# Performance work log

Measured on AMD Instinct MI355X. Metric: run time of the kernel, lower is better.

The kernel has to match this reference:

```python
import jax, jax.numpy as jnp
import numpy as np
import math

B, S, E, H, FF = 2, 2048, 768, 12, 3072
D = E // H
SCALING = 1.0
EPS = 1e-5


def layer_norm(x, g, b):
    mu = jnp.mean(x, axis=-1, keepdims=True)
    var = jnp.var(x, axis=-1, keepdims=True)
    return (x - mu) * jax.lax.rsqrt(var + EPS) * g + b


def setup_inputs() -> dict:
    key = jax.random.key(0)
    ks = jax.random.split(key, 16)
    s_e = 1.0 / math.sqrt(E)
    s_f = 1.0 / math.sqrt(FF)
    inp = {
        "x": jax.random.normal(ks[0], (B, S, E), dtype=jnp.float32),
        "Wq": jax.random.uniform(ks[1], (E, E), jnp.float32, -s_e, s_e),
        "bq": jnp.zeros((E,), jnp.float32),
        "Wk": jax.random.uniform(ks[2], (E, E), jnp.float32, -s_e, s_e),
        "bk": jnp.zeros((E,), jnp.float32),
        "Wv": jax.random.uniform(ks[3], (E, E), jnp.float32, -s_e, s_e),
        "bv": jnp.zeros((E,), jnp.float32),
        "Wo": jax.random.uniform(ks[4], (E, E), jnp.float32, -s_e, s_e),
        "bo": jnp.zeros((E,), jnp.float32),
        "W1": jax.random.uniform(ks[5], (E, FF), jnp.float32, -s_e, s_e),
        "b1": jnp.zeros((FF,), jnp.float32),
        "W2": jax.random.uniform(ks[6], (FF, E), jnp.float32, -s_f, s_f),
        "b2": jnp.zeros((E,), jnp.float32),
        "g1": jnp.ones((E,), jnp.float32),
        "be1": jnp.zeros((E,), jnp.float32),
        "g2": jnp.ones((E,), jnp.float32),
        "be2": jnp.zeros((E,), jnp.float32),
    }
    return inp


def reference(x, Wq, bq, Wk, bk, Wv, bv, Wo, bo, W1, b1, W2, b2, g1, be1, g2, be2):
    # --- multi-head attention with ALiBi-style symmetric distance bias ---
    q = (x @ Wq + bq).reshape(B, S, H, D)
    k = (x @ Wk + bk).reshape(B, S, H, D)
    v = (x @ Wv + bv).reshape(B, S, H, D)
    scores = jnp.einsum("bqhd,bkhd->bhqk", q, k) / math.sqrt(D)
    pos = jnp.arange(S)
    alibi = -SCALING * jnp.abs(pos[None, :] - pos[:, None]).astype(jnp.float32)  # [S,S]
    scores = scores + alibi  # broadcast over [B,H]
    attn_map = jax.nn.softmax(scores, axis=-1)  # [B,H,S,S]
    ctx = jnp.einsum("bhqk,bkhd->bqhd", attn_map, v).reshape(B, S, E)
    attn_out = ctx @ Wo + bo
    # --- residual + norm, FFN, residual + norm (dropout = eval/identity) ---
    h = layer_norm(x + attn_out, g1, be1)
    ff = jax.nn.relu(h @ W1 + b1) @ W2 + b2
    out = layer_norm(h + ff, g2, be2)
    return (out, attn_map)
```

## Files before the change

### kernel.cpp

```cpp
#include <hip/hip_runtime.h>
#include <stdint.h>

static constexpr int cB = 2, cS = 2048, cE = 768, cH = 12, cFF = 3072, cD = 64;
static constexpr int cM = cB * cS;

typedef __bf16 bf16x8 __attribute__((ext_vector_type(8)));
typedef float f32x4 __attribute__((ext_vector_type(4)));

__device__ __forceinline__ unsigned short f2bf(float f) {
    union { float f; unsigned int u; } v; v.f = f;
    unsigned int r = v.u + 0x7fffu + ((v.u >> 16) & 1u);
    return (unsigned short)(r >> 16);
}
__device__ __forceinline__ float bf2f(unsigned short u) {
    union { unsigned int u; float f; } v; v.u = ((unsigned int)u) << 16;
    return v.f;
}

__device__ __forceinline__ void load_lds16(const unsigned short* g, unsigned short* l) {
    __builtin_amdgcn_global_load_lds(
        (const __attribute__((address_space(1))) unsigned int*)(g),
        (__attribute__((address_space(3))) unsigned int*)(l), 16, 0, 0);
}

static constexpr size_t ZTOT = 25165824;
static constexpr int ZPB = 9984;
static constexpr int ZPT = 39;

__device__ __forceinline__ void zstore_job(float* zattn, size_t j) {
    if (j < ZTOT) {
        int row  = (int)(j >> 9);
        int slot = (int)(j & 511);
        int m064 = (row & 2047) & ~63;
        int ntlo = (m064 > 120) ? ((m064 - 120) >> 7) : 0;
        int nthi = (m064 + 183) >> 7; if (nthi > 15) nthi = 15;
        int zlo = ntlo << 5;
        int span = ((nthi + 1) << 5) - zlo;
        int chunk = slot < zlo ? slot : slot + span;
        if (chunk < 512) {
            const f32x4 z4 = {0.f, 0.f, 0.f, 0.f};
            __builtin_nontemporal_store(z4, (f32x4*)zattn + ((size_t)row << 9) + chunk);
        }
    }
}

template<int BM, int BN, int EPI>
__global__ __launch_bounds__(256, 4) void gemm_nt(
    const unsigned short* __restrict__ Ab,
    const unsigned short* __restrict__ Btp,
    float* __restrict__ outF,
    float* __restrict__ outF2,
    unsigned short* __restrict__ outB,
    unsigned short* __restrict__ outB2,
    const float* __restrict__ bias0,
    const float* __restrict__ bias1,
    const float* __restrict__ bias2,
    const float* __restrict__ resid,
    float* __restrict__ zattn, int zbase, int zqs,
    int M, int N, int K, long sB)
{
    constexpr int MI = BM / 32, NI = BN / 32;
    __shared__ alignas(16) unsigned short Sh[BM * 64 + BN * 64];
    unsigned short* Al = Sh;
    unsigned short* Bl = Sh + BM * 64;
    const int tid = threadIdx.x;
    const int lane = tid & 63, wave = tid >> 6;
    const int wm = wave >> 1, wn = wave & 1;

    const int nwg  = gridDim.x * gridDim.y * gridDim.z;
    const int orig = blockIdx.x + gridDim.x * (blockIdx.y + gridDim.y * blockIdx.z);
    const int swz  = (orig & 7) * (nwg >> 3) + (orig >> 3);
    const int bx   = swz % gridDim.x;
    const int byz  = swz / gridDim.x;
    const int by   = byz % gridDim.y;
    const int bz   = byz / gridDim.y;

    const int m0 = by * BM, n0 = bx * BN;
    const int ln = lane & 15, lg = lane >> 4;
    const int sw = ln & 7;

    const unsigned short* Bt = Btp + (size_t)bz * sB;

    const size_t zb = (size_t)(zbase + orig) * ZPB;
    int zq0 = 0;

    f32x4 acc[MI][NI];
#pragma unroll
    for (int i = 0; i < MI; i++)
#pragma unroll
        for (int j = 0; j < NI; j++) acc[i][j] = (f32x4){0.f, 0.f, 0.f, 0.f};

    int kbeg = 0, kend = K;
    if constexpr (EPI == 3) { int kh = K >> 1; kbeg = bz * kh; kend = kbeg + kh; }

    for (int k0 = kbeg; k0 < kend; k0 += 64) {
        __syncthreads();
#pragma unroll
        for (int it = 0; it < BM / 32; ++it) {
            int idx = tid + it * 256;
            int r = idx >> 3, c8 = idx & 7;
            int cs = c8 ^ (r & 7);
            load_lds16(Ab + (size_t)(m0 + r) * K + k0 + cs * 8, &Al[idx * 8]);
        }
#pragma unroll
        for (int it = 0; it < BN / 32; ++it) {
            int idx = tid + it * 256;
            int r = idx >> 3, c8 = idx & 7;
            int cs = c8 ^ (r & 7);
            load_lds16(Bt + (size_t)(n0 + r) * K + k0 + cs * 8, &Bl[idx * 8]);
        }
        if (zattn) {
            for (int q = 0; q < zqs && (zq0 + q) < ZPT; ++q)
                zstore_job(zattn, zb + (size_t)(zq0 + q) * 256 + tid);
            zq0 += zqs;
        }
        __syncthreads();
#pragma unroll
        for (int ks = 0; ks < 2; ++ks) {
            bf16x8 av[MI], bv[NI];
#pragma unroll
            for (int i = 0; i < MI; i++) {
                int row = wm * (BM / 2) + 16 * i + ln;
                av[i] = *(const bf16x8*)&Al[row * 64 + ((ks * 4 + lg) ^ sw) * 8];
            }
#pragma unroll
            for (int j = 0; j < NI; j++) {
                int row = wn * (BN / 2) + 16 * j + ln;
                bv[j] = *(const bf16x8*)&Bl[row * 64 + ((ks * 4 + lg) ^ sw) * 8];
            }
#pragma unroll
            for (int i = 0; i < MI; i++)
#pragma unroll
                for (int j = 0; j < NI; j++)
                    acc[i][j] = __builtin_amdgcn_mfma_f32_16x16x32_bf16(av[i], bv[j], acc[i][j], 0, 0, 0);
        }
    }
    if (zattn) {
        for (; zq0 < ZPT; ++zq0)
            zstore_job(zattn, zb + (size_t)zq0 * 256 + tid);
    }

    if constexpr (EPI == 0) {
        if (bz < 2) {
            const float* bia = (bz == 0) ? bias0 : bias1;
#pragma unroll
            for (int i = 0; i < MI; i++)
#pragma unroll
                for (int j = 0; j < NI; j++)
#pragma unroll
                    for (int r = 0; r < 4; r++) {
                        int m = m0 + wm * (BM / 2) + 16 * i + lg * 4 + r;
                        int n = n0 + wn * (BN / 2) + 16 * j + ln;
                        float v = acc[i][j][r] + bia[n];
                        int b = m >> 11, s = m & 2047, h = n >> 6, d = n & 63;
                        outB[(size_t)bz * ((size_t)cB * cH * cS * cD) +
                             ((((size_t)b * cH + h) * cS + s) << 6) + d] = f2bf(v);
                    }
        } else {
            constexpr int TS = BM + 8;
            __syncthreads();
#pragma unroll
            for (int i = 0; i < MI; i++)
#pragma unroll
                for (int j = 0; j < NI; j++)
#pragma unroll
                    for (int r = 0; r < 4; r++) {
                        int ml = wm * (BM / 2) + 16 * i + lg * 4 + r;
                        int nl = wn * (BN / 2) + 16 * j + ln;
                        Sh[nl * TS + ml] = f2bf(acc[i][j][r] + bias2[n0 + nl]);
                    }
            __syncthreads();
            const int b = m0 >> 11, sbase = m0 & 2047;
#pragma unroll
            for (int it = 0; it < (BN * BM / 8) / 256; ++it) {
                int idx = tid + it * 256;
                int rr = idx >> 4, c8 = idx & 15;
                uint4 val = *(const uint4*)&Sh[rr * TS + c8 * 8];
                int ng = n0 + rr;
                int h = ng >> 6, d = ng & 63;
                *(uint4*)&outB2[((((size_t)b * cH + h) << 6) + d) * (size_t)cS + sbase + c8 * 8] = val;
            }
        }
    } else if constexpr (EPI == 3) {
        float* o = (bz == 0) ? outF : outF2;
#pragma unroll
        for (int i = 0; i < MI; i++) {
#pragma unroll
            for (int j = 0; j < NI; j++) {
#pragma unroll
                for (int r = 0; r < 4; r++) {
                    int m = m0 + wm * (BM / 2) + 16 * i + lg * 4 + r;
                    int n = n0 + wn * (BN / 2) + 16 * j + ln;
                    float v = acc[i][j][r];
                    if (bz == 0) v += bias0[n] + resid[(size_t)m * N + n];
                    o[(size_t)m * N + n] = v;
                }
            }
        }
    } else {
#pragma unroll
        for (int i = 0; i < MI; i++) {
#pragma unroll
            for (int j = 0; j < NI; j++) {
#pragma unroll
                for (int r = 0; r < 4; r++) {
                    int m = m0 + wm * (BM / 2) + 16 * i + lg * 4 + r;
                    int n = n0 + wn * (BN / 2) + 16 * j + ln;
                    float v = fmaxf(acc[i][j][r] + bias0[n], 0.f);
                    outB[(size_t)m * N + n] = f2bf(v);
                }
            }
        }
    }
}

__global__ __launch_bounds__(256, 2) void attn_fused(
    const unsigned short* __restrict__ Qh,
    const unsigned short* __restrict__ Kh,
    const unsigned short* __restrict__ Vt,
    float* __restrict__ attn,
    unsigned short* __restrict__ ctxb)
{
    constexpr int VS = 136;
    __shared__ alignas(16) unsigned short KVl[128 * 64];
    __shared__ alignas(16) unsigned short Pl[3 * 64 * VS];
    __shared__ float rs2[2][64];
    __shared__ float rsinv[64];

    const int tid = threadIdx.x;
    const int lane = tid & 63, wave = tid >> 6;
    const int wm = wave >> 1, wn = wave & 1;
    const int ln = lane & 15, lg = lane >> 4;
    const int sw = ln & 7;

    const int nwg  = gridDim.x * gridDim.y;
    const int orig = blockIdx.x + gridDim.x * blockIdx.y;
    const int swz  = (orig & 7) * (nwg >> 3) + (orig >> 3);
    const int m0 = (swz % gridDim.x) * 64;
    const int bh = swz / gridDim.x;

    const int nt_lo = max(0, (m0 - 120) / 128);
    const int nt_hi = min(15, (m0 + 183) / 128);

    const unsigned short* Qg = Qh + ((size_t)bh * cS + m0) * cD;
    const unsigned short* Kg = Kh + (size_t)bh * cS * cD;
    const unsigned short* Vg = Vt + (size_t)bh * cD * cS;
    float* attng = attn + (size_t)bh * cS * cS;

#pragma unroll
    for (int it = 0; it < 2; ++it) {
        int idx = tid + it * 256;
        int r = idx >> 3, c8 = idx & 7;
        int cs = c8 ^ (r & 7);
        load_lds16(Qg + r * cD + cs * 8, &KVl[idx * 8]);
    }
    __syncthreads();
    bf16x8 qf[2][2];
#pragma unroll
    for (int ks = 0; ks < 2; ++ks)
#pragma unroll
        for (int i = 0; i < 2; i++)
            qf[ks][i] = *(const bf16x8*)&KVl[(wm * 32 + 16 * i + ln) * 64 + ((ks * 4 + lg) ^ sw) * 8];

    float psum[8];
#pragma unroll
    for (int k = 0; k < 8; k++) psum[k] = 0.f;
    f32x4 oacc[2][2];
#pragma unroll
    for (int i = 0; i < 2; i++)
#pragma unroll
        for (int j = 0; j < 2; j++) oacc[i][j] = (f32x4){0.f, 0.f, 0.f, 0.f};

    for (int nt = nt_lo; nt <= nt_hi; ++nt) {
        unsigned short* Pb = &Pl[(nt - nt_lo) * 64 * VS];
        __syncthreads();
#pragma unroll
        for (int it = 0; it < 4; ++it) {
            int idx = tid + it * 256;
            int r = idx >> 3, c8 = idx & 7;
            int cs = c8 ^ (r & 7);
            load_lds16(Kg + (size_t)(nt * 128 + r) * cD + cs * 8, &KVl[idx * 8]);
        }
        __syncthreads();
        f32x4 acc[2][4];
#pragma unroll
        for (int i = 0; i < 2; i++)
#pragma unroll
            for (int j = 0; j < 4; j++) acc[i][j] = (f32x4){0.f, 0.f, 0.f, 0.f};
#pragma unroll
        for (int ks = 0; ks < 2; ++ks) {
            bf16x8 b[4];
#pragma unroll
            for (int j = 0; j < 4; j++)
                b[j] = *(const bf16x8*)&KVl[(wn * 64 + 16 * j + ln) * 64 + ((ks * 4 + lg) ^ sw) * 8];
            __builtin_amdgcn_s_setprio(1);
#pragma unroll
            for (int i = 0; i < 2; i++)
#pragma unroll
                for (int j = 0; j < 4; j++)
                    acc[i][j] = __builtin_amdgcn_mfma_f32_16x16x32_bf16(qf[ks][i], b[j], acc[i][j], 0, 0, 0);
            __builtin_amdgcn_s_setprio(0);
        }
#pragma unroll
        for (int i = 0; i < 2; i++)
#pragma unroll
            for (int j = 0; j < 4; j++)
#pragma unroll
                for (int r = 0; r < 4; r++) {
                    int mloc = wm * 32 + 16 * i + lg * 4 + r;
                    int nloc = wn * 64 + 16 * j + ln;
                    int mg = m0 + mloc, ng = nt * 128 + nloc;
                    float e = __expf(acc[i][j][r] * 0.125f - fabsf((float)(mg - ng)));
                    psum[i * 4 + r] += e;
                    Pb[mloc * VS + nloc] = f2bf(e);
                }
        __syncthreads();
#pragma unroll
        for (int it = 0; it < 4; ++it) {
            int idx = tid + it * 256;
            int r = idx >> 4, c8 = idx & 15;
            int cs = c8 ^ (r & 7);
            load_lds16(Vg + (size_t)r * cS + nt * 128 + cs * 8, &KVl[idx * 8]);
        }
        __syncthreads();
#pragma unroll
        for (int ks = 0; ks < 4; ++ks) {
            bf16x8 pa[2], vb[2];
#pragma unroll
            for (int i = 0; i < 2; i++)
                pa[i] = *(const bf16x8*)&Pb[(wm * 32 + 16 * i + ln) * VS + ks * 32 + lg * 8];
#pragma unroll
            for (int j = 0; j < 2; j++) {
                int row = wn * 32 + 16 * j + ln;
                vb[j] = *(const bf16x8*)&KVl[row * 128 + ((ks * 4 + lg) ^ sw) * 8];
            }
            __builtin_amdgcn_s_setprio(1);
#pragma unroll
            for (int i = 0; i < 2; i++)
#pragma unroll
                for (int j = 0; j < 2; j++)
                    oacc[i][j] = __builtin_amdgcn_mfma_f32_16x16x32_bf16(pa[i], vb[j], oacc[i][j], 0, 0, 0);
            __builtin_amdgcn_s_setprio(0);
        }
    }

#pragma unroll
    for (int k = 0; k < 8; k++) {
        float v = psum[k];
        v += __shfl_xor(v, 1); v += __shfl_xor(v, 2);
        v += __shfl_xor(v, 4); v += __shfl_xor(v, 8);
        psum[k] = v;
    }
    if (ln == 0) {
#pragma unroll
        for (int i = 0; i < 2; i++)
#pragma unroll
            for (int r = 0; r < 4; r++)
                rs2[wn][wm * 32 + 16 * i + lg * 4 + r] = psum[i * 4 + r];
    }
    __syncthreads();
    if (tid < 64) rsinv[tid] = 1.f / (rs2[0][tid] + rs2[1][tid]);
    __syncthreads();
    float invl[8];
#pragma unroll
    for (int i = 0; i < 2; i++)
#pragma unroll
        for (int r = 0; r < 4; r++)
            invl[i * 4 + r] = rsinv[wm * 32 + 16 * i + lg * 4 + r];

    {
        int b = bh / cH, h = bh % cH;
#pragma unroll
        for (int i = 0; i < 2; i++)
#pragma unroll
            for (int j = 0; j < 2; j++)
#pragma unroll
                for (int r = 0; r < 4; r++) {
                    int mg = m0 + wm * 32 + 16 * i + lg * 4 + r;
                    int d = wn * 32 + 16 * j + ln;
                    ctxb[((size_t)b * cS + mg) * cE + h * 64 + d] = f2bf(oacc[i][j][r] * invl[i * 4 + r]);
                }
    }
    for (int nt = nt_lo; nt <= nt_hi; ++nt) {
        const unsigned short* Pb = &Pl[(nt - nt_lo) * 64 * VS];
#pragma unroll
        for (int t = 0; t < 8; ++t) {
            int idx = t * 256 + tid;
            int row = idx >> 5, c4 = idx & 31;
            ushort4 pv = *(const ushort4*)&Pb[row * VS + c4 * 4];
            float s = rsinv[row];
            float4 o;
            o.x = bf2f(pv.x) * s; o.y = bf2f(pv.y) * s;
            o.z = bf2f(pv.z) * s; o.w = bf2f(pv.w) * s;
            *(float4*)&attng[(size_t)(m0 + row) * cS + nt * 128 + c4 * 4] = o;
        }
    }
}

template<bool WH, bool TWO>
__global__ __launch_bounds__(256) void layernorm_k(const float* __restrict__ in,
    const float* __restrict__ in2,
    const float* __restrict__ g, const float* __restrict__ be,
    float* __restrict__ outF, unsigned short* __restrict__ outB)
{
    const size_t row = blockIdx.x;
    const float* p = in + row * cE;
    const int tid = threadIdx.x;
    float x0 = p[tid], x1 = p[tid + 256], x2 = p[tid + 512];
    if constexpr (TWO) {
        const float* q = in2 + row * cE;
        x0 += q[tid]; x1 += q[tid + 256]; x2 += q[tid + 512];
    }
    float sum = x0 + x1 + x2, sq = x0 * x0 + x1 * x1 + x2 * x2;
    __shared__ float s1[4], s2[4];
    for (int o = 32; o; o >>= 1) { sum += __shfl_xor(sum, o); sq += __shfl_xor(sq, o); }
    if ((tid & 63) == 0) { s1[tid >> 6] = sum; s2[tid >> 6] = sq; }
    __syncthreads();
    sum = s1[0] + s1[1] + s1[2] + s1[3];
    sq  = s2[0] + s2[1] + s2[2] + s2[3];
    float mu = sum * (1.f / cE);
    float var = sq * (1.f / cE) - mu * mu;
    float rstd = rsqrtf(var + 1e-5f);
#pragma unroll
    for (int i = 0; i < 3; i++) {
        int c = tid + 256 * i;
        float xv = (i == 0) ? x0 : ((i == 1) ? x1 : x2);
        float y = (xv - mu) * rstd * g[c] + be[c];
        outF[row * cE + c] = y;
        if constexpr (WH) outB[row * cE + c] = f2bf(y);
    }
}

__global__ __launch_bounds__(256) void prep_all(
    const float* __restrict__ x, unsigned short* __restrict__ xb,
    const float* __restrict__ Wq, const float* __restrict__ Wk,
    const float* __restrict__ Wv, const float* __restrict__ Wo,
    const float* __restrict__ W1, const float* __restrict__ W2,
    unsigned short* __restrict__ Wqt, unsigned short* __restrict__ W1t,
    unsigned short* __restrict__ W2t)
{
    __shared__ float t[32][33];
    int bid = blockIdx.x;
    if (bid < 3072) {
        int i = bid * 256 + threadIdx.x;
        float4 v = ((const float4*)x)[i];
        ushort4 o;
        o.x = f2bf(v.x); o.y = f2bf(v.y); o.z = f2bf(v.z); o.w = f2bf(v.w);
        ((ushort4*)xb)[i] = o;
        return;
    }
    bid -= 3072;
    const float* src; unsigned short* dst; int R, C, tx, ty;
    if (bid < 2304) {
        int m = bid / 576, tt = bid - m * 576;
        src = (m == 0) ? Wq : (m == 1) ? Wk : (m == 2) ? Wv : Wo;
        dst = Wqt + (size_t)m * 589824;
        R = 768; C = 768; tx = tt % 24; ty = tt / 24;
    } else if (bid < 4608) {
        int tt = bid - 2304;
        src = W1; dst = W1t; R = 768; C = 3072; tx = tt % 96; ty = tt / 96;
    } else {
        int tt = bid - 4608;
        src = W2; dst = W2t; R = 3072; C = 768; tx = tt % 24; ty = tt / 24;
    }
    int c0 = tx * 32, r0 = ty * 32;
    int lx = threadIdx.x & 31, ly = threadIdx.x >> 5;
#pragma unroll
    for (int i = 0; i < 32; i += 8) t[ly + i][lx] = src[(size_t)(r0 + ly + i) * C + c0 + lx];
    __syncthreads();
#pragma unroll
    for (int i = 0; i < 32; i += 8) dst[(size_t)(c0 + ly + i) * R + r0 + lx] = f2bf(t[lx][ly + i]);
}

extern "C" void kernel_launch(void* const* d_in, const int* in_sizes, int n_in,
                              void* d_out, int out_size, void* d_ws, size_t ws_size,
                              hipStream_t stream)
{
    const float* x   = (const float*)d_in[0];
    const float* Wq  = (const float*)d_in[1];
    const float* bq  = (const float*)d_in[2];
    const float* Wk  = (const float*)d_in[3];
    const float* bk  = (const float*)d_in[4];
    const float* Wv  = (const float*)d_in[5];
    const float* bv  = (const float*)d_in[6];
    const float* Wo  = (const float*)d_in[7];
    const float* bo  = (const float*)d_in[8];
    const float* W1  = (const float*)d_in[9];
    const float* b1  = (const float*)d_in[10];
    const float* W2  = (const float*)d_in[11];
    const float* b2  = (const float*)d_in[12];
    const float* g1  = (const float*)d_in[13];
    const float* be1 = (const float*)d_in[14];
    const float* g2  = (const float*)d_in[15];
    const float* be2 = (const float*)d_in[16];

    float* out  = (float*)d_out;
    float* attn = out + (size_t)cB * cS * cE;

    char* ws = (char*)d_ws;
    unsigned short* xb   = (unsigned short*)(ws + 0);
    unsigned short* ctxb = xb;
    unsigned short* Wqt  = (unsigned short*)(ws + 6291456);
    unsigned short* W1t  = (unsigned short*)(ws + 11010048);
    unsigned short* W2t  = (unsigned short*)(ws + 15728640);
    unsigned short* Qh   = (unsigned short*)(ws + 20447232);
    unsigned short* Kh   = (unsigned short*)(ws + 26738688);
    unsigned short* Vt   = (unsigned short*)(ws + 33030144);
    unsigned short* ff1b = Qh;
    float* res1a = (float*)(ws + 45613056);
    float* res1b = (float*)(ws + 58195968);
    float* hf    = res1a;
    float* res2a = (float*)(ws + 58195968);
    float* res2b = (float*)(ws + 0);
    unsigned short* hb = (unsigned short*)(ws + 70778880);

    prep_all<<<9984, 256, 0, stream>>>(x, xb, Wq, Wk, Wv, Wo, W1, W2, Wqt, W1t, W2t);
    gemm_nt<128, 96, 0><<<dim3(8, 32, 3), 256, 0, stream>>>(
        xb, Wqt, nullptr, nullptr, Qh, Vt, bq, bk, bv, nullptr, attn, 0, 4,
        cM, cE, cE, 589824);
    attn_fused<<<dim3(cS / 64, cB * cH), 256, 0, stream>>>(Qh, Kh, Vt, attn, ctxb);
    gemm_nt<128, 96, 3><<<dim3(8, 32, 2), 256, 0, stream>>>(
        ctxb, Wqt + 3 * 589824, res1a, res1b, nullptr, nullptr, bo, nullptr, nullptr, x,
        attn, 768, 7, cM, cE, cE, 0);
    layernorm_k<true, true><<<cM, 256, 0, stream>>>(res1a, res1b, g1, be1, hf, hb);
    gemm_nt<128, 128, 4><<<dim3(24, 32, 1), 256, 0, stream>>>(
        hb, W1t, nullptr, nullptr, ff1b, nullptr, b1, nullptr, nullptr, nullptr,
        attn, 1280, 4, cM, cFF, cE, 0);
    gemm_nt<128, 96, 3><<<dim3(8, 32, 2), 256, 0, stream>>>(
        ff1b, W2t, res2a, res2b, nullptr, nullptr, b2, nullptr, nullptr, hf,
        attn, 2048, 2, cM, cE, cFF, 0);
    layernorm_k<false, true><<<cM, 256, 0, stream>>>(res2a, res2b, g2, be2, out, nullptr);
}
```

Measured before the change: 567.2 us.

## Vectorize layernorm and weight transpose, load Q fragments directly from global

After: 581.3 us. +2.5%, slower.

```diff
diff --git a/kernel.cpp b/kernel.cpp
--- a/kernel.cpp
+++ b/kernel.cpp
@@ -247,20 +247,12 @@
     const unsigned short* Vg = Vt + (size_t)bh * cD * cS;
     float* attng = attn + (size_t)bh * cS * cS;
 
-#pragma unroll
-    for (int it = 0; it < 2; ++it) {
-        int idx = tid + it * 256;
-        int r = idx >> 3, c8 = idx & 7;
-        int cs = c8 ^ (r & 7);
-        load_lds16(Qg + r * cD + cs * 8, &KVl[idx * 8]);
-    }
-    __syncthreads();
     bf16x8 qf[2][2];
 #pragma unroll
     for (int ks = 0; ks < 2; ++ks)
 #pragma unroll
         for (int i = 0; i < 2; i++)
-            qf[ks][i] = *(const bf16x8*)&KVl[(wm * 32 + 16 * i + ln) * 64 + ((ks * 4 + lg) ^ sw) * 8];
+            qf[ks][i] = *(const bf16x8*)&Qg[(wm * 32 + 16 * i + ln) * cD + ks * 32 + lg * 8];
 
     float psum[8];
 #pragma unroll
@@ -398,36 +390,41 @@
 }
 
 template<bool WH, bool TWO>
-__global__ __launch_bounds__(256) void layernorm_k(const float* __restrict__ in,
+__global__ __launch_bounds__(192) void layernorm_k(const float* __restrict__ in,
     const float* __restrict__ in2,
     const float* __restrict__ g, const float* __restrict__ be,
     float* __restrict__ outF, unsigned short* __restrict__ outB)
 {
     const size_t row = blockIdx.x;
-    const float* p = in + row * cE;
     const int tid = threadIdx.x;
-    float x0 = p[tid], x1 = p[tid + 256], x2 = p[tid + 512];
+    float4 x = ((const float4*)(in + row * cE))[tid];
     if constexpr (TWO) {
-        const float* q = in2 + row * cE;
-        x0 += q[tid]; x1 += q[tid + 256]; x2 += q[tid + 512];
-    }
-    float sum = x0 + x1 + x2, sq = x0 * x0 + x1 * x1 + x2 * x2;
-    __shared__ float s1[4], s2[4];
+        float4 q = ((const float4*)(in2 + row * cE))[tid];
+        x.x += q.x; x.y += q.y; x.z += q.z; x.w += q.w;
+    }
+    float sum = x.x + x.y + x.z + x.w;
+    float sq  = x.x * x.x + x.y * x.y + x.z * x.z + x.w * x.w;
+    __shared__ float s1[3], s2[3];
     for (int o = 32; o; o >>= 1) { sum += __shfl_xor(sum, o); sq += __shfl_xor(sq, o); }
     if ((tid & 63) == 0) { s1[tid >> 6] = sum; s2[tid >> 6] = sq; }
     __syncthreads();
-    sum = s1[0] + s1[1] + s1[2] + s1[3];
-    sq  = s2[0] + s2[1] + s2[2] + s2[3];
+    sum = s1[0] + s1[1] + s1[2];
+    sq  = s2[0] + s2[1] + s2[2];
     float mu = sum * (1.f / cE);
     float var = sq * (1.f / cE) - mu * mu;
     float rstd = rsqrtf(var + 1e-5f);
-#pragma unroll
-    for (int i = 0; i < 3; i++) {
-        int c = tid + 256 * i;
-        float xv = (i == 0) ? x0 : ((i == 1) ? x1 : x2);
-        float y = (xv - mu) * rstd * g[c] + be[c];
-        outF[row * cE + c] = y;
-        if constexpr (WH) outB[row * cE + c] = f2bf(y);
+    float4 gv = ((const float4*)g)[tid];
+    float4 bv = ((const float4*)be)[tid];
+    float4 y;
+    y.x = (x.x - mu) * rstd * gv.x + bv.x;
+    y.y = (x.y - mu) * rstd * gv.y + bv.y;
+    y.z = (x.z - mu) * rstd * gv.z + bv.z;
+    y.w = (x.w - mu) * rstd * gv.w + bv.w;
+    ((float4*)(outF + row * cE))[tid] = y;
+    if constexpr (WH) {
+        ushort4 o;
+        o.x = f2bf(y.x); o.y = f2bf(y.y); o.z = f2bf(y.z); o.w = f2bf(y.w);
+        ((ushort4*)(outB + row * cE))[tid] = o;
     }
 }
 
@@ -439,7 +436,7 @@
     unsigned short* __restrict__ Wqt, unsigned short* __restrict__ W1t,
     unsigned short* __restrict__ W2t)
 {
-    __shared__ float t[32][33];
+    __shared__ float t[32][65];
     int bid = blockIdx.x;
     if (bid < 3072) {
         int i = bid * 256 + threadIdx.x;
@@ -451,25 +448,36 @@
     }
     bid -= 3072;
     const float* src; unsigned short* dst; int R, C, tx, ty;
-    if (bid < 2304) {
-        int m = bid / 576, tt = bid - m * 576;
+    if (bid < 1152) {
+        int m = bid / 288, tt = bid - m * 288;
         src = (m == 0) ? Wq : (m == 1) ? Wk : (m == 2) ? Wv : Wo;
         dst = Wqt + (size_t)m * 589824;
-        R = 768; C = 768; tx = tt % 24; ty = tt / 24;
-    } else if (bid < 4608) {
+        R = 768; C = 768; tx = tt % 12; ty = tt / 12;
+    } else if (bid < 2304) {
+        int tt = bid - 1152;
+        src = W1; dst = W1t; R = 768; C = 3072; tx = tt % 48; ty = tt / 48;
+    } else {
         int tt = bid - 2304;
-        src = W1; dst = W1t; R = 768; C = 3072; tx = tt % 96; ty = tt / 96;
-    } else {
-        int tt = bid - 4608;
-        src = W2; dst = W2t; R = 3072; C = 768; tx = tt % 24; ty = tt / 24;
-    }
-    int c0 = tx * 32, r0 = ty * 32;
-    int lx = threadIdx.x & 31, ly = threadIdx.x >> 5;
-#pragma unroll
-    for (int i = 0; i < 32; i += 8) t[ly + i][lx] = src[(size_t)(r0 + ly + i) * C + c0 + lx];
+        src = W2; dst = W2t; R = 3072; C = 768; tx = tt % 12; ty = tt / 12;
+    }
+    int c0 = tx * 64, r0 = ty * 32;
+    int lx = threadIdx.x & 15, ly = threadIdx.x >> 4;
+#pragma unroll
+    for (int i = 0; i < 32; i += 16) {
+        float4 v = *(const float4*)&src[(size_t)(r0 + ly + i) * C + c0 + lx * 4];
+        t[ly + i][lx * 4 + 0] = v.x; t[ly + i][lx * 4 + 1] = v.y;
+        t[ly + i][lx * 4 + 2] = v.z; t[ly + i][lx * 4 + 3] = v.w;
+    }
     __syncthreads();
-#pragma unroll
-    for (int i = 0; i < 32; i += 8) dst[(size_t)(c0 + ly + i) * R + r0 + lx] = f2bf(t[lx][ly + i]);
+    int wy = threadIdx.x >> 2, wx = threadIdx.x & 3;
+    ushort4 o0, o1;
+    o0.x = f2bf(t[wx * 8 + 0][wy]); o0.y = f2bf(t[wx * 8 + 1][wy]);
+    o0.z = f2bf(t[wx * 8 + 2][wy]); o0.w = f2bf(t[wx * 8 + 3][wy]);
+    o1.x = f2bf(t[wx * 8 + 4][wy]); o1.y = f2bf(t[wx * 8 + 5][wy]);
+    o1.z = f2bf(t[wx * 8 + 6][wy]); o1.w = f2bf(t[wx * 8 + 7][wy]);
+    unsigned short* dp = &dst[(size_t)(c0 + wy) * R + r0 + wx * 8];
+    *(ushort4*)(dp + 0) = o0;
+    *(ushort4*)(dp + 4) = o1;
 }
 
 extern "C" void kernel_launch(void* const* d_in, const int* in_sizes, int n_in,
@@ -514,7 +522,7 @@
     float* res2b = (float*)(ws + 0);
     unsigned short* hb = (unsigned short*)(ws + 70778880);
 
-    prep_all<<<9984, 256, 0, stream>>>(x, xb, Wq, Wk, Wv, Wo, W1, W2, Wqt, W1t, W2t);
+    prep_all<<<6528, 256, 0, stream>>>(x, xb, Wq, Wk, Wv, Wo, W1, W2, Wqt, W1t, W2t);
     gemm_nt<128, 96, 0><<<dim3(8, 32, 3), 256, 0, stream>>>(
         xb, Wqt, nullptr, nullptr, Qh, Vt, bq, bk, bv, nullptr, attn, 0, 4,
         cM, cE, cE, 589824);
@@ -522,12 +530,12 @@
     gemm_nt<128, 96, 3><<<dim3(8, 32, 2), 256, 0, stream>>>(
         ctxb, Wqt + 3 * 589824, res1a, res1b, nullptr, nullptr, bo, nullptr, nullptr, x,
         attn, 768, 7, cM, cE, cE, 0);
-    layernorm_k<true, true><<<cM, 256, 0, stream>>>(res1a, res1b, g1, be1, hf, hb);
+    layernorm_k<true, true><<<cM, 192, 0, stream>>>(res1a, res1b, g1, be1, hf, hb);
     gemm_nt<128, 128, 4><<<dim3(24, 32, 1), 256, 0, stream>>>(
         hb, W1t, nullptr, nullptr, ff1b, nullptr, b1, nullptr, nullptr, nullptr,
         attn, 1280, 4, cM, cFF, cE, 0);
     gemm_nt<128, 96, 3><<<dim3(8, 32, 2), 256, 0, stream>>>(
         ff1b, W2t, res2a, res2b, nullptr, nullptr, b2, nullptr, nullptr, hf,
         attn, 2048, 2, cM, cE, cFF, 0);
-    layernorm_k<false, true><<<cM, 256, 0, stream>>>(res2a, res2b, g2, be2, out, nullptr);
-}
+    layernorm_k<false, true><<<cM, 192, 0, stream>>>(res2a, res2b, g2, be2, out, nullptr);
+}
```
